# Performance work log

Measured on AMD Instinct MI355X. Metric: run time of the kernel, lower is better.

Reference implementation:

```python
import jax, jax.numpy as jnp
import numpy as np

ALPHA = 1.0
BETA = 1.0
GAMMA = 1.0
EPS = 1e-08

D = 128      # feature / hash-code dim
N = 4096     # number of items


def setup_inputs() -> dict:
    key = jax.random.key(0)
    k = jax.random.split(key, 6)
    return {
        "SU": jax.random.uniform(k[0], (N, N, 1), dtype=jnp.float32),
        "SP": jax.random.uniform(k[1], (N, N, 1), dtype=jnp.float32),
        "SM": jax.random.uniform(k[2], (N, N, 1), dtype=jnp.float32),
        "FP": jax.random.uniform(k[3], (D, N), dtype=jnp.float32),
        "FM": jax.random.uniform(k[4], (D, N), dtype=jnp.float32),
        "B": jax.random.uniform(k[5], (D, N), dtype=jnp.float32),
    }


def reference(SU, SP, SM, FP, FM, B):
    # IRSC: Omega_U = FP^T FM / 2, sum over all (i,j) of -S*Omega + log(1+Omega)
    omega_u = jnp.einsum('di,dj->ij', FP, FM) * 0.5          # [N, N]
    loss_irsc = jnp.sum(-SU[:, :, 0] * omega_u + jnp.log1p(omega_u))

    # IASC: same form on FP^T FP and FM^T FM, with epsilon inside the log
    omega_p = jnp.einsum('di,dj->ij', FP, FP) * 0.5
    omega_m = jnp.einsum('di,dj->ij', FM, FM) * 0.5
    loss_sp = jnp.sum(-SP[:, :, 0] * omega_p + jnp.log(1.0 + omega_p + EPS))
    loss_sm = jnp.sum(-SM[:, :, 0] * omega_m + jnp.log(1.0 + omega_m + EPS))
    loss_iasc = loss_sp + loss_sm

    # BQC: Frobenius norms (not squared)
    loss_bqc = jnp.sqrt(jnp.sum((FP - B) ** 2)) + jnp.sqrt(jnp.sum((FM - B) ** 2))

    # FDC: ||F @ ones||_F^2 = sum over rows of (row-sum)^2
    loss_fdc = jnp.sum(jnp.sum(FP, axis=1) ** 2) + jnp.sum(jnp.sum(FM, axis=1) ** 2)

    return loss_irsc + ALPHA * loss_iasc + BETA * loss_bqc + GAMMA * loss_fdc
```

## Files before the change

kernel.cpp:

```cpp
#include <hip/hip_runtime.h>
#include <hip/hip_bf16.h>
#include <math.h>

#define NN 4096
#define DD 128

typedef __attribute__((ext_vector_type(8))) short bf16x8;
typedef __attribute__((ext_vector_type(4))) float f32x4;

__global__ __launch_bounds__(256, 2)
void gemm_loss_mfma(const float* __restrict__ S, const float* __restrict__ F1,
                    const float* __restrict__ F2, float eps, double* __restrict__ accum)
{
    __shared__ char lds[2][128 * 256];
    __shared__ float red[4];
    const int t  = threadIdx.x;
    const int i0 = blockIdx.y * 128;
    const int j0 = blockIdx.x * 128;

    {
        const int il   = t & 127;
        const int half = t >> 7;
        const float* c1 = F1 + i0 + il;
        const float* c2 = F2 + j0 + il;
        char* r1 = lds[0] + il * 256;
        char* r2 = lds[1] + il * 256;
        #pragma unroll
        for (int it = 0; it < 8; ++it) {
            const int q  = half * 8 + it;
            const int d0 = q * 8;
            float a[8], b[8];
            #pragma unroll
            for (int j = 0; j < 8; ++j) {
                a[j] = c1[(long)(d0 + j) * NN];
                b[j] = c2[(long)(d0 + j) * NN];
            }
            union { __hip_bfloat162 h[4]; bf16x8 v; } pa, pb;
            #pragma unroll
            for (int j = 0; j < 4; ++j) {
                pa.h[j] = __float22bfloat162_rn(make_float2(a[2*j], a[2*j+1]));
                pb.h[j] = __float22bfloat162_rn(make_float2(b[2*j], b[2*j+1]));
            }
            const int off = (q ^ (il & 15)) << 4;
            *(bf16x8*)(r1 + off) = pa.v;
            *(bf16x8*)(r2 + off) = pb.v;
        }
    }
    __syncthreads();

    const int lane = t & 63;
    const int wid  = t >> 6;
    const int wr   = wid >> 1, wc = wid & 1;
    const int l15  = lane & 15, l4 = lane >> 4;

    float sreg[4][4][4];
    #pragma unroll
    for (int am = 0; am < 4; ++am)
        #pragma unroll
        for (int r = 0; r < 4; ++r) {
            const long gi   = (long)(i0 + wr * 64 + am * 16 + l4 * 4 + r);
            const long base = gi * NN + j0 + wc * 64 + l15;
            #pragma unroll
            for (int bn = 0; bn < 4; ++bn)
                sreg[am][bn][r] = S[base + bn * 16];
        }

    f32x4 acc[4][4] = {};
    #pragma unroll
    for (int kb = 0; kb < 4; ++kb) {
        bf16x8 af[4], bg[4];
        #pragma unroll
        for (int m = 0; m < 4; ++m) {
            const int ia = wr * 64 + m * 16 + l15;
            af[m] = *(const bf16x8*)(lds[0] + ia * 256 + (((kb * 4 + l4) ^ l15) << 4));
            const int jb = wc * 64 + m * 16 + l15;
            bg[m] = *(const bf16x8*)(lds[1] + jb * 256 + (((kb * 4 + l4) ^ l15) << 4));
        }
        #pragma unroll
        for (int m = 0; m < 4; ++m)
            #pragma unroll
            for (int n = 0; n < 4; ++n)
                acc[m][n] = __builtin_amdgcn_mfma_f32_16x16x32_bf16(af[m], bg[n], acc[m][n], 0, 0, 0);
    }

    float lsum = 0.f;
    #pragma unroll
    for (int m = 0; m < 4; ++m)
        #pragma unroll
        for (int n = 0; n < 4; ++n)
            #pragma unroll
            for (int r = 0; r < 4; ++r) {
                const float o = 0.5f * acc[m][n][r];
                lsum += fmaf(-sreg[m][n][r], o, __logf(1.0f + o + eps));
            }

    float v = lsum;
    #pragma unroll
    for (int off = 32; off; off >>= 1) v += __shfl_down(v, off);
    if ((t & 63) == 0) red[t >> 6] = v;
    __syncthreads();
    if (t == 0) {
        const float tot = red[0] + red[1] + red[2] + red[3];
        atomicAdd(accum, (double)tot);
    }
}

__global__ __launch_bounds__(256)
void bqc_kernel(const float* __restrict__ FP, const float* __restrict__ FM,
                const float* __restrict__ B, double* __restrict__ ws)
{
    __shared__ float red1[4], red2[4];
    const int n4 = DD * NN / 4;
    float s1 = 0.f, s2 = 0.f;
    for (int i = blockIdx.x * blockDim.x + threadIdx.x; i < n4;
         i += gridDim.x * blockDim.x) {
        const float4 p = ((const float4*)FP)[i];
        const float4 m = ((const float4*)FM)[i];
        const float4 b = ((const float4*)B)[i];
        float d;
        d = p.x - b.x; s1 += d * d;  d = p.y - b.y; s1 += d * d;
        d = p.z - b.z; s1 += d * d;  d = p.w - b.w; s1 += d * d;
        d = m.x - b.x; s2 += d * d;  d = m.y - b.y; s2 += d * d;
        d = m.z - b.z; s2 += d * d;  d = m.w - b.w; s2 += d * d;
    }
    const int t = threadIdx.x;
    #pragma unroll
    for (int off = 32; off; off >>= 1) {
        s1 += __shfl_down(s1, off);
        s2 += __shfl_down(s2, off);
    }
    if ((t & 63) == 0) { red1[t >> 6] = s1; red2[t >> 6] = s2; }
    __syncthreads();
    if (t == 0) {
        atomicAdd(&ws[1], (double)(red1[0] + red1[1] + red1[2] + red1[3]));
        atomicAdd(&ws[2], (double)(red2[0] + red2[1] + red2[2] + red2[3]));
    }
}

__global__ __launch_bounds__(256)
void fdc_kernel(const float* __restrict__ FP, const float* __restrict__ FM,
                double* __restrict__ ws)
{
    __shared__ float red[4];
    const float* F = (blockIdx.x >= DD) ? FM : FP;
    const int row = blockIdx.x & (DD - 1);
    float s = 0.f;
    const float4* rowp = (const float4*)&F[(long)row * NN];
    for (int i = threadIdx.x; i < NN / 4; i += blockDim.x) {
        const float4 v = rowp[i];
        s += v.x + v.y + v.z + v.w;
    }
    const int t = threadIdx.x;
    #pragma unroll
    for (int off = 32; off; off >>= 1) s += __shfl_down(s, off);
    if ((t & 63) == 0) red[t >> 6] = s;
    __syncthreads();
    if (t == 0) {
        const double rs = (double)(red[0] + red[1] + red[2] + red[3]);
        atomicAdd(&ws[3], rs * rs);
    }
}

__global__ void finalize_kernel(const double* __restrict__ ws, float* __restrict__ out)
{
    if (threadIdx.x == 0 && blockIdx.x == 0)
        out[0] = (float)(ws[0] + ws[3] + sqrt(ws[1]) + sqrt(ws[2]));
}

extern "C" void kernel_launch(void* const* d_in, const int* in_sizes, int n_in,
                              void* d_out, int out_size, void* d_ws, size_t ws_size,
                              hipStream_t stream)
{
    const float* SU = (const float*)d_in[0];
    const float* SP = (const float*)d_in[1];
    const float* SM = (const float*)d_in[2];
    const float* FP = (const float*)d_in[3];
    const float* FM = (const float*)d_in[4];
    const float* B  = (const float*)d_in[5];
    float*  out = (float*)d_out;
    double* ws  = (double*)d_ws;

    hipMemsetAsync(d_ws, 0, 4 * sizeof(double), stream);

    dim3 grid(NN / 128, NN / 128);
    gemm_loss_mfma<<<grid, 256, 0, stream>>>(SU, FP, FM, 0.0f, ws);
    gemm_loss_mfma<<<grid, 256, 0, stream>>>(SP, FP, FP, 1e-8f, ws);
    gemm_loss_mfma<<<grid, 256, 0, stream>>>(SM, FM, FM, 1e-8f, ws);
    bqc_kernel<<<512, 256, 0, stream>>>(FP, FM, B, ws);
    fdc_kernel<<<256, 256, 0, stream>>>(FP, FM, ws);
    finalize_kernel<<<1, 64, 0, stream>>>(ws, out);
}
```

Baseline: 100.9 us.

## Pre-convert F to bf16 row-major and fuse three GEMM-loss launches with async S loads

```diff
diff --git a/kernel.cpp b/kernel.cpp
--- a/kernel.cpp
+++ b/kernel.cpp
@@ -7,6 +7,118 @@
 
 typedef __attribute__((ext_vector_type(8))) short bf16x8;
 typedef __attribute__((ext_vector_type(4))) float f32x4;
+
+__device__ __forceinline__ void gload_lds16(const float* g, float* l) {
+    __builtin_amdgcn_global_load_lds((const __attribute__((address_space(1))) char*)g,
+                                     (__attribute__((address_space(3))) char*)l, 16, 0, 0);
+}
+
+__global__ __launch_bounds__(256)
+void convert_kernel(const float* __restrict__ FP, const float* __restrict__ FM,
+                    __hip_bfloat16* __restrict__ FPb, __hip_bfloat16* __restrict__ FMb)
+{
+    const float* src = blockIdx.y ? FM : FP;
+    __hip_bfloat16* dst = blockIdx.y ? FMb : FPb;
+    const int t  = threadIdx.x;
+    const int il = t & 127;
+    const int dh = t >> 7;
+    const int i  = blockIdx.x * 128 + il;
+    #pragma unroll
+    for (int it = 0; it < 8; ++it) {
+        const int d0 = dh * 64 + it * 8;
+        union { __hip_bfloat162 h[4]; bf16x8 v; } p;
+        #pragma unroll
+        for (int j = 0; j < 4; ++j) {
+            const float a = src[(long)(d0 + 2*j)     * NN + i];
+            const float b = src[(long)(d0 + 2*j + 1) * NN + i];
+            p.h[j] = __float22bfloat162_rn(make_float2(a, b));
+        }
+        *(bf16x8*)&dst[(long)i * DD + d0] = p.v;
+    }
+}
+
+__global__ __launch_bounds__(256, 2)
+void gemm_loss_mfma2(const float* __restrict__ SU, const float* __restrict__ SP,
+                     const float* __restrict__ SM,
+                     const __hip_bfloat16* __restrict__ FPb,
+                     const __hip_bfloat16* __restrict__ FMb,
+                     double* __restrict__ accum)
+{
+    __shared__ float sS[4][64 * 64];
+    __shared__ float red[4];
+    const int t    = threadIdx.x;
+    const int lane = t & 63, wid = t >> 6;
+    const int wr   = wid >> 1, wc = wid & 1;
+    const int l15  = lane & 15, l4 = lane >> 4;
+    const int z    = blockIdx.z;
+    const float* S  = (z == 0) ? SU : (z == 1) ? SP : SM;
+    const short* Fa = (const short*)((z == 2) ? FMb : FPb);
+    const short* Fb = (const short*)((z == 0) ? FMb : (z == 1) ? FPb : (const __hip_bfloat16*)FMb);
+    const float eps = (z == 0) ? 0.0f : 1e-8f;
+    const int i0 = blockIdx.y * 128;
+    const int j0 = blockIdx.x * 128;
+
+    bf16x8 af[4][4], bg[4][4];
+    {
+        const long ibase = (long)(i0 + wr * 64 + l15) * DD;
+        const long jbase = (long)(j0 + wc * 64 + l15) * DD;
+        #pragma unroll
+        for (int kb = 0; kb < 4; ++kb) {
+            const int ko = kb * 32 + l4 * 8;
+            #pragma unroll
+            for (int m = 0; m < 4; ++m) {
+                af[kb][m] = *(const bf16x8*)&Fa[ibase + (long)m * 16 * DD + ko];
+                bg[kb][m] = *(const bf16x8*)&Fb[jbase + (long)m * 16 * DD + ko];
+            }
+        }
+    }
+
+    {
+        float* qb = sS[wid];
+        const float* gb = S + (long)(i0 + wr * 64 + l4) * NN + j0 + wc * 64 + l15 * 4;
+        #pragma unroll
+        for (int q = 0; q < 16; ++q)
+            gload_lds16(gb + (long)q * 4 * NN, qb + q * 256);
+    }
+    __builtin_amdgcn_sched_barrier(0);
+
+    f32x4 acc[4][4] = {};
+    #pragma unroll
+    for (int kb = 0; kb < 4; ++kb)
+        #pragma unroll
+        for (int m = 0; m < 4; ++m)
+            #pragma unroll
+            for (int n = 0; n < 4; ++n)
+                acc[m][n] = __builtin_amdgcn_mfma_f32_16x16x32_bf16(af[kb][m], bg[kb][n], acc[m][n], 0, 0, 0);
+
+    asm volatile("s_waitcnt vmcnt(0)" ::: "memory");
+    __builtin_amdgcn_sched_barrier(0);
+
+    float lsum = 0.f;
+    const float* q = sS[wid];
+    #pragma unroll
+    for (int m = 0; m < 4; ++m)
+        #pragma unroll
+        for (int n = 0; n < 4; ++n) {
+            const int base = (m * 16 + l4 * 4) * 64 + n * 16 + l15;
+            #pragma unroll
+            for (int r = 0; r < 4; ++r) {
+                const float s = q[base + r * 64];
+                const float o = 0.5f * acc[m][n][r];
+                lsum += fmaf(-s, o, __logf(1.0f + o + eps));
+            }
+        }
+
+    float v = lsum;
+    #pragma unroll
+    for (int off = 32; off; off >>= 1) v += __shfl_down(v, off);
+    if ((t & 63) == 0) red[t >> 6] = v;
+    __syncthreads();
+    if (t == 0) {
+        const float tot = red[0] + red[1] + red[2] + red[3];
+        atomicAdd(accum, (double)tot);
+    }
+}
 
 __global__ __launch_bounds__(256, 2)
 void gemm_loss_mfma(const float* __restrict__ S, const float* __restrict__ F1,
@@ -17,7 +129,6 @@
     const int t  = threadIdx.x;
     const int i0 = blockIdx.y * 128;
     const int j0 = blockIdx.x * 128;
-
     {
         const int il   = t & 127;
         const int half = t >> 7;
@@ -47,12 +158,10 @@
         }
     }
     __syncthreads();
-
     const int lane = t & 63;
     const int wid  = t >> 6;
     const int wr   = wid >> 1, wc = wid & 1;
     const int l15  = lane & 15, l4 = lane >> 4;
-
     float sreg[4][4][4];
     #pragma unroll
     for (int am = 0; am < 4; ++am)
@@ -64,25 +173,23 @@
             for (int bn = 0; bn < 4; ++bn)
                 sreg[am][bn][r] = S[base + bn * 16];
         }
-
     f32x4 acc[4][4] = {};
     #pragma unroll
     for (int kb = 0; kb < 4; ++kb) {
-        bf16x8 af[4], bg[4];
+        bf16x8 af[4], bgr[4];
         #pragma unroll
         for (int m = 0; m < 4; ++m) {
             const int ia = wr * 64 + m * 16 + l15;
             af[m] = *(const bf16x8*)(lds[0] + ia * 256 + (((kb * 4 + l4) ^ l15) << 4));
             const int jb = wc * 64 + m * 16 + l15;
-            bg[m] = *(const bf16x8*)(lds[1] + jb * 256 + (((kb * 4 + l4) ^ l15) << 4));
+            bgr[m] = *(const bf16x8*)(lds[1] + jb * 256 + (((kb * 4 + l4) ^ l15) << 4));
         }
         #pragma unroll
         for (int m = 0; m < 4; ++m)
             #pragma unroll
             for (int n = 0; n < 4; ++n)
-                acc[m][n] = __builtin_amdgcn_mfma_f32_16x16x32_bf16(af[m], bg[n], acc[m][n], 0, 0, 0);
-    }
-
+                acc[m][n] = __builtin_amdgcn_mfma_f32_16x16x32_bf16(af[m], bgr[n], acc[m][n], 0, 0, 0);
+    }
     float lsum = 0.f;
     #pragma unroll
     for (int m = 0; m < 4; ++m)
@@ -93,7 +200,6 @@
                 const float o = 0.5f * acc[m][n][r];
                 lsum += fmaf(-sreg[m][n][r], o, __logf(1.0f + o + eps));
             }
-
     float v = lsum;
     #pragma unroll
     for (int off = 32; off; off >>= 1) v += __shfl_down(v, off);
@@ -182,10 +288,21 @@
 
     hipMemsetAsync(d_ws, 0, 4 * sizeof(double), stream);
 
-    dim3 grid(NN / 128, NN / 128);
-    gemm_loss_mfma<<<grid, 256, 0, stream>>>(SU, FP, FM, 0.0f, ws);
-    gemm_loss_mfma<<<grid, 256, 0, stream>>>(SP, FP, FP, 1e-8f, ws);
-    gemm_loss_mfma<<<grid, 256, 0, stream>>>(SM, FM, FM, 1e-8f, ws);
+    const size_t fb_bytes = (size_t)NN * DD * sizeof(__hip_bfloat16);
+    const size_t need     = 4096 + 2 * fb_bytes;
+
+    if (ws_size >= need) {
+        __hip_bfloat16* FPb = (__hip_bfloat16*)((char*)d_ws + 4096);
+        __hip_bfloat16* FMb = (__hip_bfloat16*)((char*)d_ws + 4096 + fb_bytes);
+        convert_kernel<<<dim3(NN / 128, 2), 256, 0, stream>>>(FP, FM, FPb, FMb);
+        gemm_loss_mfma2<<<dim3(NN / 128, NN / 128, 3), 256, 0, stream>>>(
+            SU, SP, SM, FPb, FMb, ws);
+    } else {
+        dim3 grid(NN / 128, NN / 128);
+        gemm_loss_mfma<<<grid, 256, 0, stream>>>(SU, FP, FM, 0.0f, ws);
+        gemm_loss_mfma<<<grid, 256, 0, stream>>>(SP, FP, FP, 1e-8f, ws);
+        gemm_loss_mfma<<<grid, 256, 0, stream>>>(SM, FM, FM, 1e-8f, ws);
+    }
     bqc_kernel<<<512, 256, 0, stream>>>(FP, FM, B, ws);
     fdc_kernel<<<256, 256, 0, stream>>>(FP, FM, ws);
     finalize_kernel<<<1, 64, 0, stream>>>(ws, out);
```

After: 98.69 us. 2.2% less time.

## Pre-convert F to bf16 and fuse three GEMM-loss passes into persistent kernel

Applied to the files above, without the earlier changes.

```diff
diff --git a/kernel.cpp b/kernel.cpp
--- a/kernel.cpp
+++ b/kernel.cpp
@@ -7,6 +7,126 @@
 
 typedef __attribute__((ext_vector_type(8))) short bf16x8;
 typedef __attribute__((ext_vector_type(4))) float f32x4;
+
+__global__ __launch_bounds__(256)
+void convert_kernel(const float* __restrict__ FP, const float* __restrict__ FM,
+                    __hip_bfloat16* __restrict__ FPb, __hip_bfloat16* __restrict__ FMb)
+{
+    const float* src = blockIdx.y ? FM : FP;
+    __hip_bfloat16* dst = blockIdx.y ? FMb : FPb;
+    const int t  = threadIdx.x;
+    const int il = t & 127;
+    const int dh = t >> 7;
+    const int i  = blockIdx.x * 128 + il;
+    #pragma unroll
+    for (int it = 0; it < 8; ++it) {
+        const int d0 = dh * 64 + it * 8;
+        union { __hip_bfloat162 h[4]; bf16x8 v; } p;
+        #pragma unroll
+        for (int j = 0; j < 4; ++j) {
+            const float a = src[(long)(d0 + 2*j)     * NN + i];
+            const float b = src[(long)(d0 + 2*j + 1) * NN + i];
+            p.h[j] = __float22bfloat162_rn(make_float2(a, b));
+        }
+        *(bf16x8*)&dst[(long)i * DD + d0] = p.v;
+    }
+}
+
+__global__ __launch_bounds__(256, 1)
+void gemm_loss_persist(const float* __restrict__ SU, const float* __restrict__ SP,
+                       const float* __restrict__ SM,
+                       const __hip_bfloat16* __restrict__ FPb_,
+                       const __hip_bfloat16* __restrict__ FMb_,
+                       double* __restrict__ accum)
+{
+    const short* FPb = (const short*)FPb_;
+    const short* FMb = (const short*)FMb_;
+    const int t0   = threadIdx.x;
+    const int lane = t0 & 63;
+    const int wid  = t0 >> 6;
+    const int l15  = lane & 15, l4 = lane >> 4;
+    const int w    = blockIdx.x * 4 + wid;
+    const int base = w * 12;
+    const int last = base + 11;
+
+    float svA[64], svB[64];
+    float lsum = 0.f;
+
+#define LOAD_S_HALF(tt, dst, mlo, mhi)                                          \
+    {                                                                           \
+        const int zz  = (tt) >> 12;                                             \
+        const int ii0 = (((tt) >> 6) & 63) << 6;                                \
+        const int jj0 = ((tt) & 63) << 6;                                       \
+        const float* Sz_ = (zz == 0) ? SU : (zz == 1) ? SP : SM;                \
+        _Pragma("unroll")                                                       \
+        for (int m = (mlo); m < (mhi); ++m)                                     \
+            _Pragma("unroll")                                                   \
+            for (int n = 0; n < 4; ++n)                                         \
+                _Pragma("unroll")                                               \
+                for (int r = 0; r < 4; ++r)                                     \
+                    dst[m*16 + n*4 + r] =                                       \
+                        Sz_[(long)(ii0 + m*16 + l4*4 + r) * NN + jj0 + n*16 + l15]; \
+    }
+
+#define ITER(tt, cur, nxt)                                                      \
+    {                                                                           \
+        const int tc = (tt);                                                    \
+        const int z  = tc >> 12;                                                \
+        const int i0 = ((tc >> 6) & 63) << 6;                                   \
+        const int j0 = (tc & 63) << 6;                                          \
+        const short* Fa = (z == 2) ? FMb : FPb;                                 \
+        const short* Fb = (z == 0) ? FMb : (z == 1) ? FPb : FMb;                \
+        const float eps = (z == 0) ? 0.0f : 1e-8f;                              \
+        bf16x8 af[4][4], bg[4][4];                                              \
+        _Pragma("unroll")                                                       \
+        for (int kb = 0; kb < 4; ++kb)                                          \
+            _Pragma("unroll")                                                   \
+            for (int m = 0; m < 4; ++m) {                                       \
+                af[kb][m] = *(const bf16x8*)&Fa[(long)(i0 + m*16 + l15) * DD + kb*32 + l4*8]; \
+                bg[kb][m] = *(const bf16x8*)&Fb[(long)(j0 + m*16 + l15) * DD + kb*32 + l4*8]; \
+            }                                                                   \
+        __builtin_amdgcn_sched_barrier(0);                                      \
+        const int tn = (tc < last) ? tc + 1 : last;                             \
+        LOAD_S_HALF(tn, nxt, 0, 2);                                             \
+        __builtin_amdgcn_sched_barrier(0);                                      \
+        f32x4 acc[4][4] = {};                                                   \
+        _Pragma("unroll")                                                       \
+        for (int kb = 0; kb < 4; ++kb)                                          \
+            _Pragma("unroll")                                                   \
+            for (int m = 0; m < 4; ++m)                                         \
+                _Pragma("unroll")                                               \
+                for (int n = 0; n < 4; ++n)                                     \
+                    acc[m][n] = __builtin_amdgcn_mfma_f32_16x16x32_bf16(af[kb][m], bg[kb][n], acc[m][n], 0, 0, 0); \
+        __builtin_amdgcn_sched_barrier(0);                                      \
+        _Pragma("unroll")                                                       \
+        for (int m = 0; m < 4; ++m)                                             \
+            _Pragma("unroll")                                                   \
+            for (int n = 0; n < 4; ++n)                                         \
+                _Pragma("unroll")                                               \
+                for (int r = 0; r < 4; ++r) {                                   \
+                    const float o = 0.5f * acc[m][n][r];                        \
+                    lsum += fmaf(-cur[m*16 + n*4 + r], o, __logf(1.0f + o + eps)); \
+                }                                                               \
+        __builtin_amdgcn_sched_barrier(0);                                      \
+        LOAD_S_HALF(tn, nxt, 2, 4);                                             \
+        __builtin_amdgcn_sched_barrier(0);                                      \
+    }
+
+    LOAD_S_HALF(base, svA, 0, 4);
+
+    #pragma unroll 1
+    for (int k = 0; k < 12; k += 2) {
+        ITER(base + k,     svA, svB);
+        ITER(base + k + 1, svB, svA);
+    }
+
+    float v = lsum;
+    #pragma unroll
+    for (int off = 32; off; off >>= 1) v += __shfl_down(v, off);
+    if (lane == 0) atomicAdd(accum, (double)v);
+#undef ITER
+#undef LOAD_S_HALF
+}
 
 __global__ __launch_bounds__(256, 2)
 void gemm_loss_mfma(const float* __restrict__ S, const float* __restrict__ F1,
@@ -17,7 +137,6 @@
     const int t  = threadIdx.x;
     const int i0 = blockIdx.y * 128;
     const int j0 = blockIdx.x * 128;
-
     {
         const int il   = t & 127;
         const int half = t >> 7;
@@ -47,42 +166,38 @@
         }
     }
     __syncthreads();
-
     const int lane = t & 63;
     const int wid  = t >> 6;
     const int wr   = wid >> 1, wc = wid & 1;
     const int l15  = lane & 15, l4 = lane >> 4;
-
     float sreg[4][4][4];
     #pragma unroll
     for (int am = 0; am < 4; ++am)
         #pragma unroll
         for (int r = 0; r < 4; ++r) {
             const long gi   = (long)(i0 + wr * 64 + am * 16 + l4 * 4 + r);
-            const long base = gi * NN + j0 + wc * 64 + l15;
+            const long basep = gi * NN + j0 + wc * 64 + l15;
             #pragma unroll
             for (int bn = 0; bn < 4; ++bn)
-                sreg[am][bn][r] = S[base + bn * 16];
+                sreg[am][bn][r] = S[basep + bn * 16];
         }
-
     f32x4 acc[4][4] = {};
     #pragma unroll
     for (int kb = 0; kb < 4; ++kb) {
-        bf16x8 af[4], bg[4];
+        bf16x8 af[4], bgr[4];
         #pragma unroll
         for (int m = 0; m < 4; ++m) {
             const int ia = wr * 64 + m * 16 + l15;
             af[m] = *(const bf16x8*)(lds[0] + ia * 256 + (((kb * 4 + l4) ^ l15) << 4));
             const int jb = wc * 64 + m * 16 + l15;
-            bg[m] = *(const bf16x8*)(lds[1] + jb * 256 + (((kb * 4 + l4) ^ l15) << 4));
+            bgr[m] = *(const bf16x8*)(lds[1] + jb * 256 + (((kb * 4 + l4) ^ l15) << 4));
         }
         #pragma unroll
         for (int m = 0; m < 4; ++m)
             #pragma unroll
             for (int n = 0; n < 4; ++n)
-                acc[m][n] = __builtin_amdgcn_mfma_f32_16x16x32_bf16(af[m], bg[n], acc[m][n], 0, 0, 0);
-    }
-
+                acc[m][n] = __builtin_amdgcn_mfma_f32_16x16x32_bf16(af[m], bgr[n], acc[m][n], 0, 0, 0);
+    }
     float lsum = 0.f;
     #pragma unroll
     for (int m = 0; m < 4; ++m)
@@ -93,7 +208,6 @@
                 const float o = 0.5f * acc[m][n][r];
                 lsum += fmaf(-sreg[m][n][r], o, __logf(1.0f + o + eps));
             }
-
     float v = lsum;
     #pragma unroll
     for (int off = 32; off; off >>= 1) v += __shfl_down(v, off);
@@ -182,10 +296,20 @@
 
     hipMemsetAsync(d_ws, 0, 4 * sizeof(double), stream);
 
-    dim3 grid(NN / 128, NN / 128);
-    gemm_loss_mfma<<<grid, 256, 0, stream>>>(SU, FP, FM, 0.0f, ws);
-    gemm_loss_mfma<<<grid, 256, 0, stream>>>(SP, FP, FP, 1e-8f, ws);
-    gemm_loss_mfma<<<grid, 256, 0, stream>>>(SM, FM, FM, 1e-8f, ws);
+    const size_t fb_bytes = (size_t)NN * DD * sizeof(__hip_bfloat16);
+    const size_t need     = 4096 + 2 * fb_bytes;
+
+    if (ws_size >= need) {
+        __hip_bfloat16* FPb = (__hip_bfloat16*)((char*)d_ws + 4096);
+        __hip_bfloat16* FMb = (__hip_bfloat16*)((char*)d_ws + 4096 + fb_bytes);
+        convert_kernel<<<dim3(NN / 128, 2), 256, 0, stream>>>(FP, FM, FPb, FMb);
+        gemm_loss_persist<<<256, 256, 0, stream>>>(SU, SP, SM, FPb, FMb, ws);
+    } else {
+        dim3 grid(NN / 128, NN / 128);
+        gemm_loss_mfma<<<grid, 256, 0, stream>>>(SU, FP, FM, 0.0f, ws);
+        gemm_loss_mfma<<<grid, 256, 0, stream>>>(SP, FP, FP, 1e-8f, ws);
+        gemm_loss_mfma<<<grid, 256, 0, stream>>>(SM, FM, FM, 1e-8f, ws);
+    }
     bqc_kernel<<<512, 256, 0, stream>>>(FP, FM, B, ws);
     fdc_kernel<<<256, 256, 0, stream>>>(FP, FM, ws);
     finalize_kernel<<<1, 64, 0, stream>>>(ws, out);
```

Measured after the change: 122.6 us. 1.21x slower.
